# Performance work log

Measured on AMD Instinct MI355X. Metric: run time of the kernel, lower is better.

Reference implementation:

```python
import jax, jax.numpy as jnp
import numpy as np

BIG = 1e10
RADIUS = 0.5
NSAMPLE = 1


def square_distance(src, dst):
    # src: [B,N,3], dst: [B,M,3] -> [B,N,M] squared euclidean distances
    d = -2.0 * jnp.einsum('bnc,bmc->bnm', src, dst)
    d = d + jnp.sum(src ** 2, -1)[:, :, None]
    d = d + jnp.sum(dst ** 2, -1)[:, None, :]
    return d


def farthest_point_sample(xyz, npoint):
    # xyz: [B,N,3]; returns int32 indices [B,npoint]
    B, N, _ = xyz.shape
    dist0 = jnp.full((B, N), BIG, dtype=xyz.dtype)
    far0 = jnp.argmax(xyz[:, :, 0], axis=1).astype(jnp.int32)

    def step(carry, _):
        dist, far = carry
        centroid = jnp.take_along_axis(xyz, far[:, None, None], axis=1)  # [B,1,3]
        d = jnp.sum((xyz - centroid) ** 2, -1)  # [B,N]
        dist = jnp.minimum(dist, d)
        new_far = jnp.argmax(dist, axis=-1).astype(jnp.int32)
        return (dist, new_far), far  # record PRE-update farthest, like the torch loop

    (_, _), centroids = jax.lax.scan(step, (dist0, far0), None, length=npoint)
    return centroids.T  # [B,npoint]


def index_points(points, idx):
    # points: [B,N,C], idx: [B,S] -> [B,S,C]
    return jnp.take_along_axis(points, idx[:, :, None], axis=1)


def query_ball_point(radius, nsample, xyz, new_xyz):
    # xyz: [B,N,3], new_xyz: [B,S,3] -> int32 [B,S,nsample]
    B, S, _ = new_xyz.shape
    N = xyz.shape[1]
    sqrdists = square_distance(new_xyz, xyz)  # [B,S,N]
    base = jnp.arange(N, dtype=jnp.int32)
    group_idx = jnp.where(sqrdists > radius ** 2, jnp.int32(N), base)  # [B,S,N]
    group_idx = jnp.sort(group_idx, axis=-1)[:, :, :nsample]
    group_first = jnp.broadcast_to(group_idx[:, :, :1], group_idx.shape)
    group_idx = jnp.where(group_idx == N, group_first, group_idx)
    return group_idx


def setup_inputs() -> dict:
    key = jax.random.key(0)
    k1, k2 = jax.random.split(key)
    B, N = 4, 16384
    xyz = jax.random.uniform(k1, (B, 3, N), dtype=jnp.float32)
    cls_label = jax.random.uniform(k2, (B, 16), dtype=jnp.float32)
    return {"xyz": xyz, "cls_label": cls_label, "npoint": 1024}


def reference(xyz, cls_label, npoint):
    pts = jnp.transpose(xyz, (0, 2, 1))  # [B,N,3]
    centroids = farthest_point_sample(pts, npoint)  # [B,S]
    new_xyz = index_points(pts, centroids)  # [B,S,3]
    idx = query_ball_point(RADIUS, NSAMPLE, pts, new_xyz)  # [B,S,1]
    return idx
```

## Files before the change

kernel.cpp:

```cpp
#include <hip/hip_runtime.h>


constexpr int N_PTS  = 16384;
constexpr int NPOINT = 1024;
constexpr int BLOCK  = 512;
constexpr int KPT    = N_PTS / BLOCK;
constexpr int NWAVE  = BLOCK / 64;

__device__ inline unsigned long long pack_key(float v, int idx) {
    return ((unsigned long long)__float_as_uint(v) << 32) |
           (unsigned)(N_PTS - 1 - idx);
}
__device__ inline int key_idx(unsigned long long k) {
    return N_PTS - 1 - (int)(k & 0xFFFFu);
}
__device__ inline unsigned long long umax64(unsigned long long a,
                                            unsigned long long b) {
    return a > b ? a : b;
}

template <int CTRL, int RM, int BM>
__device__ inline unsigned long long dpp_max_step(unsigned long long key) {
    const int lo = (int)(unsigned)key;
    const int hi = (int)(unsigned)(key >> 32);
    const unsigned mlo =
        (unsigned)__builtin_amdgcn_update_dpp(lo, lo, CTRL, RM, BM, false);
    const unsigned mhi =
        (unsigned)__builtin_amdgcn_update_dpp(hi, hi, CTRL, RM, BM, false);
    const unsigned long long moved = ((unsigned long long)mhi << 32) | mlo;
    return key > moved ? key : moved;
}

__device__ inline unsigned long long wave_max_key(unsigned long long key) {
    key = dpp_max_step<0x111, 0xf, 0xf>(key);
    key = dpp_max_step<0x112, 0xf, 0xf>(key);
    key = dpp_max_step<0x114, 0xf, 0xe>(key);
    key = dpp_max_step<0x118, 0xf, 0xc>(key);
    key = dpp_max_step<0x142, 0xa, 0xf>(key);
    key = dpp_max_step<0x143, 0xc, 0xf>(key);
    return key;
}

__global__ __launch_bounds__(BLOCK)
__attribute__((amdgpu_waves_per_eu(2, 2))) void fps_kernel(
    const float* __restrict__ xyz,
    int* __restrict__ cent)
{
    const int b   = blockIdx.x;
    const int tid = threadIdx.x;
    const float* X = xyz + (size_t)b * 3 * N_PTS;
    const float* Y = X + N_PTS;
    const float* Z = X + 2 * N_PTS;

    float px[KPT], py[KPT], pz[KPT], dst[KPT];
#pragma unroll
    for (int k = 0; k < KPT; ++k) {
        const int p = tid + k * BLOCK;
        px[k] = X[p];
        py[k] = Y[p];
        pz[k] = Z[p];
        dst[k] = 1e10f;
    }
#pragma unroll
    for (int k = 0; k < KPT; ++k)
        asm volatile("" : "+v"(px[k]), "+v"(py[k]), "+v"(pz[k]));

    __shared__ unsigned long long s_key[2][NWAVE];

    const int wave = tid >> 6;
    const int lane = tid & 63;

    int far;
    {
        float bv = px[0];
        int   bi = tid;
#pragma unroll
        for (int k = 1; k < KPT; ++k) {
            if (px[k] > bv) { bv = px[k]; bi = tid + k * BLOCK; }
        }
        const unsigned long long key = wave_max_key(pack_key(bv, bi));
        if (lane == 63) s_key[0][wave] = key;
        __syncthreads();
        const unsigned long long* sk = s_key[0];
        const unsigned long long bkk =
            umax64(umax64(umax64(sk[0], sk[1]), umax64(sk[2], sk[3])),
                   umax64(umax64(sk[4], sk[5]), umax64(sk[6], sk[7])));
        far = __builtin_amdgcn_readfirstlane(key_idx(bkk)) &
              (N_PTS - 1);
    }

    for (int it = 0; it < NPOINT; ++it) {
        if (tid == 0) cent[b * NPOINT + it] = far;
        if (it == NPOINT - 1) break;

        const float cx = X[far];
        const float cy = Y[far];
        const float cz = Z[far];

        float nbv = -1.0f;
        int   nbi = 0;
#pragma unroll
        for (int k = 0; k < KPT; ++k) {
            const float dx = __fsub_rn(px[k], cx);
            const float dy = __fsub_rn(py[k], cy);
            const float dz = __fsub_rn(pz[k], cz);
            const float d  = __fadd_rn(
                __fadd_rn(__fmul_rn(dx, dx), __fmul_rn(dy, dy)),
                __fmul_rn(dz, dz));
            const float nd = fminf(dst[k], d);
            dst[k] = nd;
            if (nd > nbv) { nbv = nd; nbi = tid + k * BLOCK; }
        }

        const unsigned long long key = wave_max_key(pack_key(nbv, nbi));
        const int buf = (it + 1) & 1;
        if (lane == 63) s_key[buf][wave] = key;
        __syncthreads();

        const unsigned long long* sk = s_key[buf];
        const unsigned long long bkk =
            umax64(umax64(umax64(sk[0], sk[1]), umax64(sk[2], sk[3])),
                   umax64(umax64(sk[4], sk[5]), umax64(sk[6], sk[7])));
        far = __builtin_amdgcn_readfirstlane(key_idx(bkk)) &
              (N_PTS - 1);
    }
}

__global__ __launch_bounds__(256) void ballq_kernel(
    const float* __restrict__ xyz,
    const int* __restrict__ cent,
    int* __restrict__ out)
{
    const int gw   = (blockIdx.x * 256 + threadIdx.x) >> 6;
    const int lane = threadIdx.x & 63;
    const int b = gw / NPOINT;
    const int s = gw % NPOINT;

    const float* X = xyz + (size_t)b * 3 * N_PTS;
    const float* Y = X + N_PTS;
    const float* Z = X + 2 * N_PTS;

    const int ci = cent[b * NPOINT + s] & (N_PTS - 1);
    const float cx = X[ci];
    const float cy = Y[ci];
    const float cz = Z[ci];
    const float cn = __fadd_rn(
        __fadd_rn(__fmul_rn(cx, cx), __fmul_rn(cy, cy)), __fmul_rn(cz, cz));

    int res = N_PTS;
    for (int base = 0; base < N_PTS; base += 64) {
        const int p = base + lane;
        const float x = X[p];
        const float y = Y[p];
        const float z = Z[p];
        const float dot = __fadd_rn(
            __fadd_rn(__fmul_rn(x, cx), __fmul_rn(y, cy)), __fmul_rn(z, cz));
        const float pn = __fadd_rn(
            __fadd_rn(__fmul_rn(x, x), __fmul_rn(y, y)), __fmul_rn(z, z));
        const float d = __fadd_rn(__fadd_rn(__fmul_rn(-2.0f, dot), cn), pn);
        const bool hit = !(d > 0.25f);
        const unsigned long long m = __ballot(hit);
        if (m) {
            res = base + (__ffsll((long long)m) - 1);
            break;
        }
    }
    if (lane == 0) out[b * NPOINT + s] = res;
}

extern "C" void kernel_launch(void* const* d_in, const int* in_sizes, int n_in,
                              void* d_out, int out_size, void* d_ws, size_t ws_size,
                              hipStream_t stream) {
    const float* xyz = (const float*)d_in[0];
    const int B = in_sizes[1] / 16;
    int* cent = (int*)d_ws;
    int* out  = (int*)d_out;

    fps_kernel<<<B, BLOCK, 0, stream>>>(xyz, cent);

    const int nwaves  = B * NPOINT;
    const int nblocks = nwaves / 4;
    ballq_kernel<<<nblocks, 256, 0, stream>>>(xyz, cent, out);
}
```

Measured before the change: 1.730 ms.

## Morton-sort points and skip FPS distance updates via per-thread bounding boxes

Adds a pre-pass that bins points into a 16^3 Morton grid using a shared-memory histogram and prefix scan. Each FPS thread then owns a spatially compact, contiguous run of points and keeps their bounding box. Per iteration, a wave skips the distance-update loop when every lane's box lower bound to the new centroid is at least its current max distance, so its cached key stays valid. This removes most of the FPS arithmetic, at the cost of an extra kernel, workspace use, and per-point index loads from sidx inside the loop.

```diff
diff --git a/kernel.cpp b/kernel.cpp
--- a/kernel.cpp
+++ b/kernel.cpp
@@ -6,6 +6,8 @@
 constexpr int BLOCK  = 512;
 constexpr int KPT    = N_PTS / BLOCK;
 constexpr int NWAVE  = BLOCK / 64;
+constexpr int NCELL  = 4096;
+constexpr int BPT    = NCELL / BLOCK;
 
 __device__ inline unsigned long long pack_key(float v, int idx) {
     return ((unsigned long long)__float_as_uint(v) << 32) |
@@ -30,7 +32,6 @@
     const unsigned long long moved = ((unsigned long long)mhi << 32) | mlo;
     return key > moved ? key : moved;
 }
-
 __device__ inline unsigned long long wave_max_key(unsigned long long key) {
     key = dpp_max_step<0x111, 0xf, 0xf>(key);
     key = dpp_max_step<0x112, 0xf, 0xf>(key);
@@ -41,29 +42,97 @@
     return key;
 }
 
+__device__ inline unsigned part4(unsigned v) {
+    return (v & 1u) | ((v & 2u) << 2) | ((v & 4u) << 4) | ((v & 8u) << 6);
+}
+
+__global__ __launch_bounds__(BLOCK) void sort_kernel(
+    const float* __restrict__ xyz, float* __restrict__ sdat)
+{
+    const int b = blockIdx.x, tid = threadIdx.x;
+    const float* X = xyz + (size_t)b * 3 * N_PTS;
+    const float* Y = X + N_PTS;
+    const float* Z = X + 2 * N_PTS;
+    float* sx = sdat + (size_t)b * 4 * N_PTS;
+    float* sy = sx + N_PTS;
+    float* sz = sy + N_PTS;
+    int*   sidx = (int*)(sz + N_PTS);
+
+    __shared__ int hist[NCELL];
+    __shared__ int part[BLOCK];
+    for (int i = tid; i < NCELL; i += BLOCK) hist[i] = 0;
+    __syncthreads();
+
+    int code[KPT];
+#pragma unroll
+    for (int k = 0; k < KPT; ++k) {
+        const int p = tid + k * BLOCK;
+        const int cx = min(15, max(0, (int)(X[p] * 16.0f)));
+        const int cy = min(15, max(0, (int)(Y[p] * 16.0f)));
+        const int cz = min(15, max(0, (int)(Z[p] * 16.0f)));
+        code[k] = (int)(part4(cx) | (part4(cy) << 1) | (part4(cz) << 2));
+        atomicAdd(&hist[code[k]], 1);
+    }
+    __syncthreads();
+
+    int loc[BPT], s = 0;
+#pragma unroll
+    for (int j = 0; j < BPT; ++j) { loc[j] = hist[tid * BPT + j]; s += loc[j]; }
+    part[tid] = s;
+    __syncthreads();
+    for (int off = 1; off < BLOCK; off <<= 1) {
+        const int v = (tid >= off) ? part[tid - off] : 0;
+        __syncthreads();
+        part[tid] += v;
+        __syncthreads();
+    }
+    int run = part[tid] - s;
+#pragma unroll
+    for (int j = 0; j < BPT; ++j) { const int c = loc[j]; hist[tid * BPT + j] = run; run += c; }
+    __syncthreads();
+
+#pragma unroll
+    for (int k = 0; k < KPT; ++k) {
+        const int p = tid + k * BLOCK;
+        const int pos = atomicAdd(&hist[code[k]], 1);
+        sx[pos] = X[p];
+        sy[pos] = Y[p];
+        sz[pos] = Z[p];
+        sidx[pos] = p;
+    }
+}
+
 __global__ __launch_bounds__(BLOCK)
 __attribute__((amdgpu_waves_per_eu(2, 2))) void fps_kernel(
     const float* __restrict__ xyz,
-    int* __restrict__ cent)
+    const float* __restrict__ sdat,
+    int* __restrict__ cent,
+    int use_sorted)
 {
     const int b   = blockIdx.x;
     const int tid = threadIdx.x;
     const float* X = xyz + (size_t)b * 3 * N_PTS;
     const float* Y = X + N_PTS;
     const float* Z = X + 2 * N_PTS;
+    const float* sx = sdat + (size_t)b * 4 * N_PTS;
+    const float* sy = sx + N_PTS;
+    const float* sz = sy + N_PTS;
+    const int* sidx = (const int*)(sz + N_PTS);
+    const int base = tid * KPT;
 
     float px[KPT], py[KPT], pz[KPT], dst[KPT];
+    float bnx =  1e30f, bny =  1e30f, bnz =  1e30f;
+    float bxx = -1e30f, bxy = -1e30f, bxz = -1e30f;
 #pragma unroll
     for (int k = 0; k < KPT; ++k) {
-        const int p = tid + k * BLOCK;
-        px[k] = X[p];
-        py[k] = Y[p];
-        pz[k] = Z[p];
+        float x, y, z;
+        if (use_sorted) { x = sx[base + k]; y = sy[base + k]; z = sz[base + k]; }
+        else { const int p = tid + k * BLOCK; x = X[p]; y = Y[p]; z = Z[p]; }
+        px[k] = x; py[k] = y; pz[k] = z;
+        bnx = fminf(bnx, x); bny = fminf(bny, y); bnz = fminf(bnz, z);
+        bxx = fmaxf(bxx, x); bxy = fmaxf(bxy, y); bxz = fmaxf(bxz, z);
         dst[k] = 1e10f;
     }
-#pragma unroll
-    for (int k = 0; k < KPT; ++k)
-        asm volatile("" : "+v"(px[k]), "+v"(py[k]), "+v"(pz[k]));
 
     __shared__ unsigned long long s_key[2][NWAVE];
 
@@ -72,22 +141,25 @@
 
     int far;
     {
-        float bv = px[0];
-        int   bi = tid;
-#pragma unroll
-        for (int k = 1; k < KPT; ++k) {
-            if (px[k] > bv) { bv = px[k]; bi = tid + k * BLOCK; }
+        unsigned long long tk = 0ull;
+#pragma unroll
+        for (int k = 0; k < KPT; ++k) {
+            const int id = use_sorted ? sidx[base + k] : tid + k * BLOCK;
+            tk = umax64(tk, pack_key(px[k], id));
         }
-        const unsigned long long key = wave_max_key(pack_key(bv, bi));
+        const unsigned long long key = wave_max_key(tk);
         if (lane == 63) s_key[0][wave] = key;
         __syncthreads();
         const unsigned long long* sk = s_key[0];
         const unsigned long long bkk =
             umax64(umax64(umax64(sk[0], sk[1]), umax64(sk[2], sk[3])),
                    umax64(umax64(sk[4], sk[5]), umax64(sk[6], sk[7])));
-        far = __builtin_amdgcn_readfirstlane(key_idx(bkk)) &
-              (N_PTS - 1);
-    }
+        far = __builtin_amdgcn_readfirstlane(key_idx(bkk)) & (N_PTS - 1);
+    }
+
+    float bv = 1e10f;
+    unsigned long long tkey = 0ull;
+    unsigned long long wkey = 0ull;
 
     for (int it = 0; it < NPOINT; ++it) {
         if (tid == 0) cent[b * NPOINT + it] = far;
@@ -97,32 +169,40 @@
         const float cy = Y[far];
         const float cz = Z[far];
 
-        float nbv = -1.0f;
-        int   nbi = 0;
-#pragma unroll
-        for (int k = 0; k < KPT; ++k) {
-            const float dx = __fsub_rn(px[k], cx);
-            const float dy = __fsub_rn(py[k], cy);
-            const float dz = __fsub_rn(pz[k], cz);
-            const float d  = __fadd_rn(
-                __fadd_rn(__fmul_rn(dx, dx), __fmul_rn(dy, dy)),
-                __fmul_rn(dz, dz));
-            const float nd = fminf(dst[k], d);
-            dst[k] = nd;
-            if (nd > nbv) { nbv = nd; nbi = tid + k * BLOCK; }
+        const float tx = fmaxf(fmaxf(bnx - cx, cx - bxx), 0.0f);
+        const float ty = fmaxf(fmaxf(bny - cy, cy - bxy), 0.0f);
+        const float tz = fmaxf(fmaxf(bnz - cz, cz - bxz), 0.0f);
+        const float lb = tx * tx + ty * ty + tz * tz;
+        const bool nosck = (lb * 0.999f >= bv);
+
+        if (!__all((int)nosck)) {
+            unsigned long long tk = 0ull;
+#pragma unroll
+            for (int k = 0; k < KPT; ++k) {
+                const float dx = __fsub_rn(px[k], cx);
+                const float dy = __fsub_rn(py[k], cy);
+                const float dz = __fsub_rn(pz[k], cz);
+                const float d  = __fadd_rn(
+                    __fadd_rn(__fmul_rn(dx, dx), __fmul_rn(dy, dy)),
+                    __fmul_rn(dz, dz));
+                const float nd = fminf(dst[k], d);
+                dst[k] = nd;
+                const int id = use_sorted ? sidx[base + k] : tid + k * BLOCK;
+                tk = umax64(tk, pack_key(nd, id));
+            }
+            tkey = tk;
+            bv = __uint_as_float((unsigned)(tkey >> 32));
+            wkey = wave_max_key(tkey);
         }
-
-        const unsigned long long key = wave_max_key(pack_key(nbv, nbi));
         const int buf = (it + 1) & 1;
-        if (lane == 63) s_key[buf][wave] = key;
+        if (lane == 63) s_key[buf][wave] = wkey;
         __syncthreads();
 
         const unsigned long long* sk = s_key[buf];
         const unsigned long long bkk =
             umax64(umax64(umax64(sk[0], sk[1]), umax64(sk[2], sk[3])),
                    umax64(umax64(sk[4], sk[5]), umax64(sk[6], sk[7])));
-        far = __builtin_amdgcn_readfirstlane(key_idx(bkk)) &
-              (N_PTS - 1);
+        far = __builtin_amdgcn_readfirstlane(key_idx(bkk)) & (N_PTS - 1);
     }
 }
 
@@ -174,9 +254,15 @@
     const float* xyz = (const float*)d_in[0];
     const int B = in_sizes[1] / 16;
     int* cent = (int*)d_ws;
-    int* out  = (int*)d_out;
-
-    fps_kernel<<<B, BLOCK, 0, stream>>>(xyz, cent);
+    const size_t cent_bytes = (size_t)B * NPOINT * 4;
+    float* sdat = (float*)((char*)d_ws + cent_bytes);
+    const size_t need = cent_bytes + (size_t)B * 4 * N_PTS * 4;
+    const int use_sorted = (ws_size >= need) ? 1 : 0;
+    int* out = (int*)d_out;
+
+    if (use_sorted)
+        sort_kernel<<<B, BLOCK, 0, stream>>>(xyz, sdat);
+    fps_kernel<<<B, BLOCK, 0, stream>>>(xyz, sdat, cent, use_sorted);
 
     const int nwaves  = B * NPOINT;
     const int nblocks = nwaves / 4;
```

Result: slower. 3.789 ms (+119.1%).
